# Kernel tuning notes

Measured on AMD Instinct MI355X. Metric: run time of the kernel, lower is better.

Reference implementation:

```python
import jax, jax.numpy as jnp
import numpy as np

N, NFEAT, NHID, NCLASS, NHEADS = 4096, 512, 64, 40, 8
ALPHA = 0.2  # LeakyReLU negative slope
NEG_BIG = -9e15


def _xavier(key, shape, gain=1.414):
    fan_in, fan_out = shape[0], shape[1]
    bound = gain * np.sqrt(6.0 / (fan_in + fan_out))
    return jax.random.uniform(key, shape, jnp.float32, -bound, bound)


def setup_inputs() -> dict:
    key = jax.random.key(0)
    ks = jax.random.split(key, 6)
    x = jax.random.normal(ks[0], (N, NFEAT), jnp.float32)
    adj = jax.random.randint(ks[1], (N, N), 0, 2).astype(jnp.float32)
    # per-head params of the 8 input GAT layers
    Ws = _xavier(ks[2], (NHEADS, NFEAT, NHID))          # stacked W: [H, F, D]
    a_s = _xavier(ks[3], (NHEADS, 2 * NHID, 1))[..., 0]  # [H, 2D]
    # output GAT layer (concat=False)
    W_out = _xavier(ks[4], (NHID * NHEADS, NCLASS))
    a_out = _xavier(ks[5], (2 * NCLASS, 1))[..., 0]      # [2C]
    return {"x": x, "adj": adj, "Ws": Ws, "a_s": a_s, "W_out": W_out, "a_out": a_out}


def _gat_layer(inp, adj_mask, W, a, concat):
    # h = inp @ W : [N, D]
    h = inp @ W
    D = h.shape[1]
    a1, a2 = a[:D], a[D:]
    # e[i,j] = leakyrelu(a . [h_i, h_j]) = leakyrelu(h_i.a1 + h_j.a2)
    # (same math as the N*N*2D concat in the original, without materializing it)
    f1 = h @ a1  # [N]
    f2 = h @ a2  # [N]
    e = jax.nn.leaky_relu(f1[:, None] + f2[None, :], negative_slope=ALPHA)
    att = jax.nn.softmax(jnp.where(adj_mask, e, NEG_BIG), axis=1)
    h_prime = att @ h  # [N, D]
    return jax.nn.elu(h_prime) if concat else h_prime


def reference(x, adj, Ws, a_s, W_out, a_out):
    adj_mask = adj > 0
    # 8 attention heads over the input features (eval mode: dropout is identity)
    heads = jax.vmap(lambda W, a: _gat_layer(x, adj_mask, W, a, True))(Ws, a_s)  # [H, N, D]
    x2 = jnp.transpose(heads, (1, 0, 2)).reshape(N, NHEADS * NHID)  # concat along feature dim
    out = _gat_layer(x2, adj_mask, W_out, a_out, False)  # [N, C]
    out = jax.nn.elu(out)
    return jax.nn.log_softmax(out, axis=1)
```

## Files before the change

### kernel.cpp

```cpp
#include <hip/hip_runtime.h>
#include <hip/hip_bf16.h>
#include <stdint.h>

#define NN 4096
#define NF 512
#define NH 64
#define NCLS 40
#define NHEADS 8
#define LOG2E 1.4426950408889634f

typedef __attribute__((ext_vector_type(8))) short bh8;
typedef __attribute__((ext_vector_type(4))) float f32x4;

__device__ __forceinline__ unsigned short f2bu(float f) {
    union { float f; unsigned u; } v; v.f = f;
    unsigned r = (v.u + 0x7FFFu + ((v.u >> 16) & 1u)) >> 16;
    return (unsigned short)r;
}
__device__ __forceinline__ float lrelu(float x) { return fmaxf(x, 0.2f * x); }
__device__ __forceinline__ float elu1(float x) { return x > 0.f ? x : expm1f(x); }
__device__ __forceinline__ float exp2fast(float x) {
    float r; asm("v_exp_f32 %0, %1" : "=v"(r) : "v"(x)); return r;
}
__device__ __forceinline__ unsigned fenc(float f) {
    unsigned u = __builtin_bit_cast(unsigned, f);
    return ((int)u < 0) ? ~u : (u | 0x80000000u);
}
__device__ __forceinline__ float fdec(unsigned k) {
    unsigned u = (k & 0x80000000u) ? (k ^ 0x80000000u) : ~k;
    return __builtin_bit_cast(float, u);
}
__device__ __forceinline__ int sbfe1(unsigned v, int off) {
#if __has_builtin(__builtin_amdgcn_sbfe)
    return __builtin_amdgcn_sbfe((int)v, off, 1);
#else
    return ((int)(v << (31 - off))) >> 31;
#endif
}
__device__ __forceinline__ float bmask(float p, unsigned mdw, int bit) {
    return __builtin_bit_cast(float,
        __builtin_bit_cast(unsigned, p) & (unsigned)sbfe1(mdw, bit));
}
__device__ __forceinline__ unsigned pack2(float x, float y) {
    unsigned ux = __builtin_bit_cast(unsigned, x), uy = __builtin_bit_cast(unsigned, y);
    ux += 0x7FFFu + ((ux >> 16) & 1u);
    uy += 0x7FFFu + ((uy >> 16) & 1u);
    return __builtin_amdgcn_perm(uy, ux, 0x07060302u);
}

__global__ __launch_bounds__(256) void prep_all_k(const float* __restrict__ x,
                                                  const float* __restrict__ adj,
                                                  const float* __restrict__ Ws,
                                                  const float* __restrict__ Wo,
                                                  unsigned short* __restrict__ xb,
                                                  unsigned short* __restrict__ WT,
                                                  unsigned short* __restrict__ WoT,
                                                  unsigned char* __restrict__ adjp,
                                                  unsigned* __restrict__ FM1u,
                                                  unsigned* __restrict__ FM2u) {
    const int bid = blockIdx.x, tid = threadIdx.x;
    if (bid < 8192) {
        __shared__ unsigned char sm[4][64];
        const int i = bid >> 1, half = bid & 1;
        const float* rp = adj + (size_t)i * NN + half * 2048 + tid * 8;
        float4 v0 = ((const float4*)rp)[0];
        float4 v1 = ((const float4*)rp)[1];
        unsigned b = (v0.x > 0.f ? 1u : 0u) | (v0.y > 0.f ? 2u : 0u) |
                     (v0.z > 0.f ? 4u : 0u) | (v0.w > 0.f ? 8u : 0u) |
                     (v1.x > 0.f ? 16u : 0u) | (v1.y > 0.f ? 32u : 0u) |
                     (v1.z > 0.f ? 64u : 0u) | (v1.w > 0.f ? 128u : 0u);
        sm[tid & 3][tid >> 2] = (unsigned char)b;
        __syncthreads();
        if (tid < 64) {
            int gp = tid >> 4, word = tid & 15;
            unsigned d = *(const unsigned*)&sm[gp][word * 4];
            *(unsigned*)(adjp + ((size_t)i * 4 + gp) * 128 + half * 64 + word * 4) = d;
        }
    } else if (bid < 10240) {
        if (bid == 8192) {
            if (tid < 8) FM1u[tid] = 0u;
            if (tid == 8) FM2u[0] = 0u;
        }
        int t = (bid - 8192) * 256 + tid;
        float4 v = ((const float4*)x)[t];
        uint2 o; o.x = pack2(v.x, v.y); o.y = pack2(v.z, v.w);
        ((uint2*)xb)[t] = o;
    } else if (bid < 11264) {
        int j = (bid - 10240) * 256 + tid;
        int c = j >> 9, k = j & 511;
        WT[j] = f2bu(Ws[(size_t)(c >> 6) * (NF * NH) + (size_t)k * NH + (c & 63)]);
    } else {
        int j = (bid - 11264) * 256 + tid;
        int c = j >> 9, k = j & 511;
        WoT[j] = f2bu(c < NCLS ? Wo[(size_t)k * NCLS + c] : 0.f);
    }
}

__global__ __launch_bounds__(512) void gemm1_k(const unsigned short* __restrict__ xb,
                                               const unsigned short* __restrict__ WT,
                                               const float* __restrict__ a_s,
                                               unsigned short* __restrict__ Bp1,
                                               float* __restrict__ f1L,
                                               float* __restrict__ f2L,
                                               unsigned* __restrict__ FM1u) {
    __shared__ unsigned short xs[128 * 40];
    __shared__ unsigned short wsm[64 * 40];
    const int tid = threadIdx.x;
    const int w = tid >> 6, lane = tid & 63, r16 = lane & 15, grp = lane >> 4;
    const int i0 = blockIdx.x << 7, h = blockIdx.y, c0 = h << 6;
    const int srow = tid >> 2, sseg = tid & 3;
    const unsigned short* xsrc = xb + (size_t)(i0 + srow) * NF + sseg * 8;
    const unsigned short* wsrc = WT + (size_t)(c0 + (srow & 63)) * NF + sseg * 8;
    f32x4 a0 = {0,0,0,0}, a1 = {0,0,0,0}, a2 = {0,0,0,0}, a3 = {0,0,0,0};
    bh8 rx = *(const bh8*)(xsrc);
    bh8 rw; if (tid < 256) rw = *(const bh8*)(wsrc);
    for (int kb = 0; kb < NF; kb += 32) {
        *(bh8*)(xs + srow * 40 + sseg * 8) = rx;
        if (tid < 256) *(bh8*)(wsm + srow * 40 + sseg * 8) = rw;
        __syncthreads();
        if (kb + 32 < NF) {
            rx = *(const bh8*)(xsrc + kb + 32);
            if (tid < 256) rw = *(const bh8*)(wsrc + kb + 32);
        }
        bh8 af = *(const bh8*)(xs + (w * 16 + r16) * 40 + grp * 8);
        bh8 b0 = *(const bh8*)(wsm + (r16) * 40 + grp * 8);
        bh8 b1 = *(const bh8*)(wsm + (16 + r16) * 40 + grp * 8);
        bh8 b2 = *(const bh8*)(wsm + (32 + r16) * 40 + grp * 8);
        bh8 b3 = *(const bh8*)(wsm + (48 + r16) * 40 + grp * 8);
        a0 = __builtin_amdgcn_mfma_f32_16x16x32_bf16(af, b0, a0, 0, 0, 0);
        a1 = __builtin_amdgcn_mfma_f32_16x16x32_bf16(af, b1, a1, 0, 0, 0);
        a2 = __builtin_amdgcn_mfma_f32_16x16x32_bf16(af, b2, a2, 0, 0, 0);
        a3 = __builtin_amdgcn_mfma_f32_16x16x32_bf16(af, b3, a3, 0, 0, 0);
        __syncthreads();
    }
    const int jt = (i0 >> 5) + (w >> 1);
    const int kg = ((w & 1) << 1) + (grp >> 1);
    const int lanep = kg * 16 + r16;
    const int ebase = (grp & 1) * 4;
    unsigned short* bp = Bp1 + ((size_t)(h * 128 + jt)) * 2048 + lanep * 8 + ebase;
    {
        uint2 v;
        v.x = pack2(a0[0], a0[1]); v.y = pack2(a0[2], a0[3]); *(uint2*)(bp + 0 * 512) = v;
        v.x = pack2(a1[0], a1[1]); v.y = pack2(a1[2], a1[3]); *(uint2*)(bp + 1 * 512) = v;
        v.x = pack2(a2[0], a2[1]); v.y = pack2(a2[2], a2[3]); *(uint2*)(bp + 2 * 512) = v;
        v.x = pack2(a3[0], a3[1]); v.y = pack2(a3[2], a3[3]); *(uint2*)(bp + 3 * 512) = v;
    }
    const float* ap = a_s + h * 128;
    float a1v[4], a2v[4];
#pragma unroll
    for (int n = 0; n < 4; ++n) { a1v[n] = ap[r16 + 16 * n]; a2v[n] = ap[64 + r16 + 16 * n]; }
    float wmax = -3.0e38f;
#pragma unroll
    for (int r = 0; r < 4; ++r) {
        const int orow = i0 + w * 16 + grp * 4 + r;
        float s1 = a0[r] * a1v[0] + a1[r] * a1v[1] + a2[r] * a1v[2] + a3[r] * a1v[3];
        float s2 = a0[r] * a2v[0] + a1[r] * a2v[1] + a2[r] * a2v[2] + a3[r] * a2v[3];
#pragma unroll
        for (int o2 = 1; o2 < 16; o2 <<= 1) { s1 += __shfl_xor(s1, o2); s2 += __shfl_xor(s2, o2); }
        s1 *= LOG2E; s2 *= LOG2E;
        if (r16 == 0) { f1L[h * NN + orow] = s1; f2L[h * NN + orow] = s2; }
        wmax = fmaxf(wmax, s2);
    }
    wmax = fmaxf(wmax, __shfl_xor(wmax, 16));
    wmax = fmaxf(wmax, __shfl_xor(wmax, 32));
    if (lane == 0) atomicMax(&FM1u[h], fenc(wmax));
}

__global__ __launch_bounds__(256) void gemm2_k(const unsigned short* __restrict__ x2b,
                                               const unsigned short* __restrict__ WoT,
                                               const float* __restrict__ a_out,
                                               unsigned short* __restrict__ Bp2,
                                               float* __restrict__ f12L,
                                               float* __restrict__ f22L,
                                               unsigned* __restrict__ FM2u) {
    __shared__ unsigned short xs[64 * 40];
    __shared__ unsigned short wsm[48 * 40];
    const int tid = threadIdx.x;
    const int w = tid >> 6, lane = tid & 63, r16 = lane & 15, grp = lane >> 4;
    const int i0 = blockIdx.x << 6;
    const int srow = tid >> 2, sseg = tid & 3;
    const unsigned short* xsrc = x2b + (size_t)(i0 + srow) * NF + sseg * 8;
    const unsigned short* wsrc = WoT + (size_t)srow * NF + sseg * 8;
    f32x4 a0 = {0,0,0,0}, a1 = {0,0,0,0}, a2 = {0,0,0,0};
    bh8 rx = *(const bh8*)(xsrc);
    bh8 rw; if (tid < 192) rw = *(const bh8*)(wsrc);
    for (int kb = 0; kb < NF; kb += 32) {
        *(bh8*)(xs + srow * 40 + sseg * 8) = rx;
        if (tid < 192) *(bh8*)(wsm + srow * 40 + sseg * 8) = rw;
        __syncthreads();
        if (kb + 32 < NF) {
            rx = *(const bh8*)(xsrc + kb + 32);
            if (tid < 192) rw = *(const bh8*)(wsrc + kb + 32);
        }
        bh8 af = *(const bh8*)(xs + (w * 16 + r16) * 40 + grp * 8);
        bh8 b0 = *(const bh8*)(wsm + (r16) * 40 + grp * 8);
        bh8 b1 = *(const bh8*)(wsm + (16 + r16) * 40 + grp * 8);
        bh8 b2 = *(const bh8*)(wsm + (32 + r16) * 40 + grp * 8);
        a0 = __builtin_amdgcn_mfma_f32_16x16x32_bf16(af, b0, a0, 0, 0, 0);
        a1 = __builtin_amdgcn_mfma_f32_16x16x32_bf16(af, b1, a1, 0, 0, 0);
        a2 = __builtin_amdgcn_mfma_f32_16x16x32_bf16(af, b2, a2, 0, 0, 0);
        __syncthreads();
    }
    const int jt = (i0 >> 5) + (w >> 1);
    const int kg = ((w & 1) << 1) + (grp >> 1);
    const int lanep = kg * 16 + r16;
    const int ebase = (grp & 1) * 4;
    unsigned short* bp = Bp2 + (size_t)jt * 1536 + lanep * 8 + ebase;
    {
        uint2 v;
        v.x = pack2(a0[0], a0[1]); v.y = pack2(a0[2], a0[3]); *(uint2*)(bp + 0 * 512) = v;
        v.x = pack2(a1[0], a1[1]); v.y = pack2(a1[2], a1[3]); *(uint2*)(bp + 1 * 512) = v;
        v.x = pack2(a2[0], a2[1]); v.y = pack2(a2[2], a2[3]); *(uint2*)(bp + 2 * 512) = v;
    }
    float a1v[3], a2v[3];
#pragma unroll
    for (int n = 0; n < 3; ++n) {
        int col = r16 + 16 * n;
        a1v[n] = col < NCLS ? a_out[col] : 0.f;
        a2v[n] = col < NCLS ? a_out[NCLS + col] : 0.f;
    }
    float wmax = -3.0e38f;
#pragma unroll
    for (int r = 0; r < 4; ++r) {
        const int orow = i0 + w * 16 + grp * 4 + r;
        float s1 = a0[r] * a1v[0] + a1[r] * a1v[1] + a2[r] * a1v[2];
        float s2 = a0[r] * a2v[0] + a1[r] * a2v[1] + a2[r] * a2v[2];
#pragma unroll
        for (int o2 = 1; o2 < 16; o2 <<= 1) { s1 += __shfl_xor(s1, o2); s2 += __shfl_xor(s2, o2); }
        s1 *= LOG2E; s2 *= LOG2E;
        if (r16 == 0) { f12L[orow] = s1; f22L[orow] = s2; }
        wmax = fmaxf(wmax, s2);
    }
    wmax = fmaxf(wmax, __shfl_xor(wmax, 16));
    wmax = fmaxf(wmax, __shfl_xor(wmax, 32));
    if (lane == 0) atomicMax(&FM2u[0], fenc(wmax));
}

__global__ __launch_bounds__(512, 4) void attn1_k(const unsigned short* __restrict__ Bp1,
                                                  const unsigned char* __restrict__ adjp,
                                                  const float* __restrict__ f1L,
                                                  const float* __restrict__ f2L,
                                                  const unsigned* __restrict__ FM1u,
                                                  unsigned short* __restrict__ x2b) {
    __shared__ float EFs[8192];
    __shared__ unsigned ADJd[64 * 4 * 33];
    const int tid = threadIdx.x, w = tid >> 6, lane = tid & 63;
    const int r16 = lane & 15, grp = lane >> 4;
    const int rowg = w & 3, jq = w >> 2;
    const int h = blockIdx.y;
    const int i0 = blockIdx.x * 64;
    const float fm = fdec(FM1u[h]);
    const float* f2p = f2L + h * NN;
    for (int t = 0; t < 8; ++t) {
        int j = tid + t * 512;
        float d = f2p[j] - fm;
        EFs[2 * j] = exp2fast(d);
        EFs[2 * j + 1] = exp2fast(0.2f * d);
    }
    {
        const unsigned* asrc = (const unsigned*)(adjp + (size_t)i0 * 512);
        for (int t = 0; t < 16; ++t) {
            int idx = tid + t * 512;
            ADJd[(idx >> 5) * 33 + (idx & 31)] = asrc[idx];
        }
    }
    const int irow = i0 + rowg * 16 + r16;
    const float f1v = f1L[h * NN + irow];
    const float mL = lrelu(f1v + fm);
    const float A = exp2fast(f1v + fm - mL);
    const float B = exp2fast(__builtin_fmaf(0.2f, f1v + fm, -mL));
    __syncthreads();
    const unsigned* adjrd = ADJd + ((rowg * 16 + r16) * 4 + grp) * 33 + jq * 16;
    const float* efp = EFs + grp * 16;
    const unsigned short* Bbase = Bp1 + (size_t)h * 128 * 2048 + lane * 8;
    f32x4 acc0 = {0,0,0,0}, acc1 = {0,0,0,0}, acc2 = {0,0,0,0}, acc3 = {0,0,0,0}, accd = {0,0,0,0};
    const short ov = (r16 == 0) ? (short)0x3F80 : (short)0;
    bh8 ones;
#pragma unroll
    for (int e = 0; e < 8; ++e) ones[e] = ov;
    bh8 nb0, nb1, nb2, nb3;
#define PREF1(JT) { const unsigned short* Bn = Bbase + (size_t)(JT) * 2048;              \
        nb0 = *(const bh8*)(Bn);        nb1 = *(const bh8*)(Bn + 512);                    \
        nb2 = *(const bh8*)(Bn + 1024); nb3 = *(const bh8*)(Bn + 1536); }
    const int jtbase = jq * 64;
    PREF1(jtbase);
    for (int jt4 = 0; jt4 < 16; ++jt4) {
        const unsigned mdw = adjrd[jt4];
#pragma unroll
        for (int u = 0; u < 4; ++u) {
            const int jt = jtbase + jt4 * 4 + u;
            bh8 b0 = nb0, b1 = nb1, b2 = nb2, b3 = nb3;
            PREF1(jt + 1);
            const float* e4 = efp + jt * 64;
            float4 ea = *(const float4*)(e4);
            float4 eb = *(const float4*)(e4 + 4);
            float4 ec = *(const float4*)(e4 + 8);
            float4 ed = *(const float4*)(e4 + 12);
            const int bb = u * 8;
            union { bh8 v; unsigned u32[4]; } pk;
            {
                float p0 = bmask(fmaxf(A * ea.x, B * ea.y), mdw, bb + 0);
                float p1 = bmask(fmaxf(A * ea.z, B * ea.w), mdw, bb + 1);
                pk.u32[0] = __builtin_amdgcn_perm(__builtin_bit_cast(unsigned, p1),
                                                  __builtin_bit_cast(unsigned, p0), 0x07060302u);
                float p2 = bmask(fmaxf(A * eb.x, B * eb.y), mdw, bb + 2);
                float p3 = bmask(fmaxf(A * eb.z, B * eb.w), mdw, bb + 3);
                pk.u32[1] = __builtin_amdgcn_perm(__builtin_bit_cast(unsigned, p3),
                                                  __builtin_bit_cast(unsigned, p2), 0x07060302u);
                float p4 = bmask(fmaxf(A * ec.x, B * ec.y), mdw, bb + 4);
                float p5 = bmask(fmaxf(A * ec.z, B * ec.w), mdw, bb + 5);
                pk.u32[2] = __builtin_amdgcn_perm(__builtin_bit_cast(unsigned, p5),
                                                  __builtin_bit_cast(unsigned, p4), 0x07060302u);
                float p6 = bmask(fmaxf(A * ed.x, B * ed.y), mdw, bb + 6);
                float p7 = bmask(fmaxf(A * ed.z, B * ed.w), mdw, bb + 7);
                pk.u32[3] = __builtin_amdgcn_perm(__builtin_bit_cast(unsigned, p7),
                                                  __builtin_bit_cast(unsigned, p6), 0x07060302u);
            }
            acc0 = __builtin_amdgcn_mfma_f32_16x16x32_bf16(pk.v, b0, acc0, 0, 0, 0);
            acc1 = __builtin_amdgcn_mfma_f32_16x16x32_bf16(pk.v, b1, acc1, 0, 0, 0);
            acc2 = __builtin_amdgcn_mfma_f32_16x16x32_bf16(pk.v, b2, acc2, 0, 0, 0);
            acc3 = __builtin_amdgcn_mfma_f32_16x16x32_bf16(pk.v, b3, acc3, 0, 0, 0);
            accd = __builtin_amdgcn_mfma_f32_16x16x32_bf16(pk.v, ones, accd, 0, 0, 0);
        }
    }
#undef PREF1
    __syncthreads();
    float (*comb)[64][21] = (float(*)[64][21])EFs;
    if (jq == 1) {
        float* cb = &comb[rowg][lane][0];
#pragma unroll
        for (int r = 0; r < 4; ++r) {
            cb[r] = acc0[r]; cb[4 + r] = acc1[r]; cb[8 + r] = acc2[r];
            cb[12 + r] = acc3[r]; cb[16 + r] = accd[r];
        }
    }
    __syncthreads();
    if (jq == 0) {
        const float* cb = &comb[rowg][lane][0];
#pragma unroll
        for (int r = 0; r < 4; ++r) {
            acc0[r] += cb[r]; acc1[r] += cb[4 + r]; acc2[r] += cb[8 + r];
            acc3[r] += cb[12 + r]; accd[r] += cb[16 + r];
        }
#pragma unroll
        for (int r = 0; r < 4; ++r) {
            const float den = __shfl(accd[r], lane & 48);
            const float inv = 1.0f / den;
            unsigned short* o = x2b + (size_t)(i0 + rowg * 16 + grp * 4 + r) * NF + h * 64 + r16;
            o[0]  = f2bu(elu1(acc0[r] * inv));
            o[16] = f2bu(elu1(acc1[r] * inv));
            o[32] = f2bu(elu1(acc2[r] * inv));
            o[48] = f2bu(elu1(acc3[r] * inv));
        }
    }
}

__global__ __launch_bounds__(512, 6) void attn2_k(const unsigned short* __restrict__ Bp2,
                                                  const unsigned char* __restrict__ adjp,
                                                  const float* __restrict__ f12L,
                                                  const float* __restrict__ f22L,
                                                  const unsigned* __restrict__ FM2u,
                                                  float* __restrict__ out) {
    __shared__ float EFs[8192];
    __shared__ float comb[8][64][17];
    const int tid = threadIdx.x, w = tid >> 6, lane = tid & 63;
    const int r16 = lane & 15, grp = lane >> 4;
    const int i0 = blockIdx.x * 16;
    const int i = i0 + r16;
    const float fm = fdec(FM2u[0]);
    for (int t = 0; t < 8; ++t) {
        int j = tid + t * 512;
        float d = f22L[j] - fm;
        EFs[2 * j] = exp2fast(d);
        EFs[2 * j + 1] = exp2fast(0.2f * d);
    }
    const float f1v = f12L[i];
    const float mL = lrelu(f1v + fm);
    const float A = exp2fast(f1v + fm - mL);
    const float B = exp2fast(__builtin_fmaf(0.2f, f1v + fm, -mL));
    __syncthreads();
    const int jt0 = w * 16;
    const uint4 a4 = *(const uint4*)(adjp + ((size_t)i * 4 + grp) * 128 + jt0);
    f32x4 acc0 = {0,0,0,0}, acc1 = {0,0,0,0}, acc2 = {0,0,0,0}, accd = {0,0,0,0};
    const short ov = (r16 == 0) ? (short)0x3F80 : (short)0;
    bh8 ones;
#pragma unroll
    for (int e = 0; e < 8; ++e) ones[e] = ov;
    const unsigned short* Bbase = Bp2 + lane * 8;
    const float* efp = EFs + grp * 16;
    bh8 nb0, nb1, nb2;
#define PREF2(JT) { const unsigned short* Bn = Bbase + (size_t)(JT) * 1536;              \
        nb0 = *(const bh8*)(Bn); nb1 = *(const bh8*)(Bn + 512); nb2 = *(const bh8*)(Bn + 1024); }
    PREF2(jt0);
#pragma unroll
    for (int q = 0; q < 4; ++q) {
        const unsigned mdw = (q == 0) ? a4.x : (q == 1) ? a4.y : (q == 2) ? a4.z : a4.w;
#pragma unroll
        for (int u = 0; u < 4; ++u) {
            const int jt = jt0 + q * 4 + u;
            bh8 b0 = nb0, b1 = nb1, b2 = nb2;
            PREF2(jt + 1);
            const float* e4 = efp + jt * 64;
            float4 ea = *(const float4*)(e4);
            float4 eb = *(const float4*)(e4 + 4);
            float4 ec = *(const float4*)(e4 + 8);
            float4 ed = *(const float4*)(e4 + 12);
            const int bb = u * 8;
            union { bh8 v; unsigned u32[4]; } pk;
            {
                float p0 = bmask(fmaxf(A * ea.x, B * ea.y), mdw, bb + 0);
                float p1 = bmask(fmaxf(A * ea.z, B * ea.w), mdw, bb + 1);
                pk.u32[0] = __builtin_amdgcn_perm(__builtin_bit_cast(unsigned, p1),
                                                  __builtin_bit_cast(unsigned, p0), 0x07060302u);
                float p2 = bmask(fmaxf(A * eb.x, B * eb.y), mdw, bb + 2);
                float p3 = bmask(fmaxf(A * eb.z, B * eb.w), mdw, bb + 3);
                pk.u32[1] = __builtin_amdgcn_perm(__builtin_bit_cast(unsigned, p3),
                                                  __builtin_bit_cast(unsigned, p2), 0x07060302u);
                float p4 = bmask(fmaxf(A * ec.x, B * ec.y), mdw, bb + 4);
                float p5 = bmask(fmaxf(A * ec.z, B * ec.w), mdw, bb + 5);
                pk.u32[2] = __builtin_amdgcn_perm(__builtin_bit_cast(unsigned, p5),
                                                  __builtin_bit_cast(unsigned, p4), 0x07060302u);
                float p6 = bmask(fmaxf(A * ed.x, B * ed.y), mdw, bb + 6);
                float p7 = bmask(fmaxf(A * ed.z, B * ed.w), mdw, bb + 7);
                pk.u32[3] = __builtin_amdgcn_perm(__builtin_bit_cast(unsigned, p7),
                                                  __builtin_bit_cast(unsigned, p6), 0x07060302u);
            }
            acc0 = __builtin_amdgcn_mfma_f32_16x16x32_bf16(pk.v, b0, acc0, 0, 0, 0);
            acc1 = __builtin_amdgcn_mfma_f32_16x16x32_bf16(pk.v, b1, acc1, 0, 0, 0);
            acc2 = __builtin_amdgcn_mfma_f32_16x16x32_bf16(pk.v, b2, acc2, 0, 0, 0);
            accd = __builtin_amdgcn_mfma_f32_16x16x32_bf16(pk.v, ones, accd, 0, 0, 0);
        }
    }
#undef PREF2
    {
        float* cb = &comb[w][lane][0];
#pragma unroll
        for (int r = 0; r < 4; ++r) {
            cb[r] = acc0[r]; cb[4 + r] = acc1[r]; cb[8 + r] = acc2[r]; cb[12 + r] = accd[r];
        }
    }
    __syncthreads();
    if (w < 4) {
        const float* sb = &comb[w + 4][lane][0];
        float* cb = &comb[w][lane][0];
#pragma unroll
        for (int r = 0; r < 4; ++r) {
            acc0[r] += sb[r]; acc1[r] += sb[4 + r]; acc2[r] += sb[8 + r]; accd[r] += sb[12 + r];
            cb[r] = acc0[r]; cb[4 + r] = acc1[r]; cb[8 + r] = acc2[r]; cb[12 + r] = accd[r];
        }
    }
    __syncthreads();
    if (w < 2) {
        const float* sb = &comb[w + 2][lane][0];
        float* cb = &comb[w][lane][0];
#pragma unroll
        for (int r = 0; r < 4; ++r) {
            acc0[r] += sb[r]; acc1[r] += sb[4 + r]; acc2[r] += sb[8 + r]; accd[r] += sb[12 + r];
            cb[r] = acc0[r]; cb[4 + r] = acc1[r]; cb[8 + r] = acc2[r]; cb[12 + r] = accd[r];
        }
    }
    __syncthreads();
    if (w == 0) {
        const float* sb = &comb[1][lane][0];
#pragma unroll
        for (int r = 0; r < 4; ++r) {
            acc0[r] += sb[r]; acc1[r] += sb[4 + r]; acc2[r] += sb[8 + r]; accd[r] += sb[12 + r];
        }
#pragma unroll
        for (int r = 0; r < 4; ++r) {
            const int row = grp * 4 + r;
            const float den = __shfl(accd[r], lane & 48);
            const float inv = 1.0f / den;
            float v0 = elu1(acc0[r] * inv);
            float v1 = elu1(acc1[r] * inv);
            float v2 = (r16 < 8) ? elu1(acc2[r] * inv) : -3.0e38f;
            float mx = fmaxf(fmaxf(v0, v1), v2);
#pragma unroll
            for (int o = 1; o < 16; o <<= 1) mx = fmaxf(mx, __shfl_xor(mx, o));
            float ex = __expf(v0 - mx) + __expf(v1 - mx) + ((r16 < 8) ? __expf(v2 - mx) : 0.f);
#pragma unroll
            for (int o = 1; o < 16; o <<= 1) ex += __shfl_xor(ex, o);
            const float lse = mx + logf(ex);
            float* op = out + (size_t)(i0 + row) * NCLS;
            op[r16] = v0 - lse;
            op[16 + r16] = v1 - lse;
            if (r16 < 8) op[32 + r16] = v2 - lse;
        }
    }
}

#define OFF_XB   0ULL
#define OFF_WT   4194304ULL
#define OFF_WOT  4718592ULL
#define OFF_BP1  4767744ULL
#define OFF_X2B  8962048ULL
#define OFF_BP2  13156352ULL
#define OFF_F1L  13549568ULL
#define OFF_F2L  13680640ULL
#define OFF_F12  13811712ULL
#define OFF_F22  13828096ULL
#define OFF_FM1  13844480ULL
#define OFF_FM2  13844736ULL
#define OFF_ADJ  13844992ULL

extern "C" void kernel_launch(void* const* d_in, const int* in_sizes, int n_in,
                              void* d_out, int out_size, void* d_ws, size_t ws_size,
                              hipStream_t stream) {
    const float* x     = (const float*)d_in[0];
    const float* adj   = (const float*)d_in[1];
    const float* Ws    = (const float*)d_in[2];
    const float* a_s   = (const float*)d_in[3];
    const float* W_out = (const float*)d_in[4];
    const float* a_out = (const float*)d_in[5];
    float* out = (float*)d_out;
    char* w = (char*)d_ws;

    unsigned short* xb  = (unsigned short*)(w + OFF_XB);
    unsigned short* WT  = (unsigned short*)(w + OFF_WT);
    unsigned short* WoT = (unsigned short*)(w + OFF_WOT);
    unsigned short* Bp1 = (unsigned short*)(w + OFF_BP1);
    unsigned short* x2b = (unsigned short*)(w + OFF_X2B);
    unsigned short* Bp2 = (unsigned short*)(w + OFF_BP2);
    float* f1L = (float*)(w + OFF_F1L);
    float* f2L = (float*)(w + OFF_F2L);
    float* f12 = (float*)(w + OFF_F12);
    float* f22 = (float*)(w + OFF_F22);
    unsigned* FM1u = (unsigned*)(w + OFF_FM1);
    unsigned* FM2u = (unsigned*)(w + OFF_FM2);
    unsigned char* adjp = (unsigned char*)(w + OFF_ADJ);

    prep_all_k<<<11360, 256, 0, stream>>>(x, adj, Ws, W_out, xb, WT, WoT, adjp, FM1u, FM2u);
    gemm1_k<<<dim3(32, 8), 512, 0, stream>>>(xb, WT, a_s, Bp1, f1L, f2L, FM1u);
    attn1_k<<<dim3(64, 8), 512, 0, stream>>>(Bp1, adjp, f1L, f2L, FM1u, x2b);
    gemm2_k<<<64, 256, 0, stream>>>(x2b, WoT, a_out, Bp2, f12, f22, FM2u);
    attn2_k<<<256, 512, 0, stream>>>(Bp2, adjp, f12, f22, FM2u, out);
}
```

Baseline: 195.1 us.

## Double-buffer GEMM shared tiles, deepen attention B prefetch, widen adj packing

Both GEMM kernels now use double-buffered shared-memory tiles. The next K-slice is written into the alternate buffer after the MFMAs, which removes one barrier per iteration. The attention kernel prefetches B fragments two tiles ahead using alternating register sets, aiming to hide more global latency at the cost of extra registers. The adjacency bit-packing now handles a full row per block with 16 floats per thread, halving the block count of the prep kernel.

```diff
diff --git a/kernel.cpp b/kernel.cpp
--- a/kernel.cpp
+++ b/kernel.cpp
@@ -59,38 +59,45 @@
                                                   unsigned* __restrict__ FM1u,
                                                   unsigned* __restrict__ FM2u) {
     const int bid = blockIdx.x, tid = threadIdx.x;
-    if (bid < 8192) {
-        __shared__ unsigned char sm[4][64];
-        const int i = bid >> 1, half = bid & 1;
-        const float* rp = adj + (size_t)i * NN + half * 2048 + tid * 8;
+    if (bid < 4096) {
+        __shared__ unsigned char sm[4][128];
+        const int i = bid;
+        const float* rp = adj + (size_t)i * NN + tid * 16;
         float4 v0 = ((const float4*)rp)[0];
         float4 v1 = ((const float4*)rp)[1];
-        unsigned b = (v0.x > 0.f ? 1u : 0u) | (v0.y > 0.f ? 2u : 0u) |
-                     (v0.z > 0.f ? 4u : 0u) | (v0.w > 0.f ? 8u : 0u) |
-                     (v1.x > 0.f ? 16u : 0u) | (v1.y > 0.f ? 32u : 0u) |
-                     (v1.z > 0.f ? 64u : 0u) | (v1.w > 0.f ? 128u : 0u);
-        sm[tid & 3][tid >> 2] = (unsigned char)b;
+        float4 v2 = ((const float4*)rp)[2];
+        float4 v3 = ((const float4*)rp)[3];
+        unsigned b0 = (v0.x > 0.f ? 1u : 0u) | (v0.y > 0.f ? 2u : 0u) |
+                      (v0.z > 0.f ? 4u : 0u) | (v0.w > 0.f ? 8u : 0u) |
+                      (v1.x > 0.f ? 16u : 0u) | (v1.y > 0.f ? 32u : 0u) |
+                      (v1.z > 0.f ? 64u : 0u) | (v1.w > 0.f ? 128u : 0u);
+        unsigned b1 = (v2.x > 0.f ? 1u : 0u) | (v2.y > 0.f ? 2u : 0u) |
+                      (v2.z > 0.f ? 4u : 0u) | (v2.w > 0.f ? 8u : 0u) |
+                      (v3.x > 0.f ? 16u : 0u) | (v3.y > 0.f ? 32u : 0u) |
+                      (v3.z > 0.f ? 64u : 0u) | (v3.w > 0.f ? 128u : 0u);
+        sm[(tid & 1) * 2][tid >> 1] = (unsigned char)b0;
+        sm[(tid & 1) * 2 + 1][tid >> 1] = (unsigned char)b1;
         __syncthreads();
-        if (tid < 64) {
-            int gp = tid >> 4, word = tid & 15;
+        if (tid < 128) {
+            int gp = tid >> 5, word = tid & 31;
             unsigned d = *(const unsigned*)&sm[gp][word * 4];
-            *(unsigned*)(adjp + ((size_t)i * 4 + gp) * 128 + half * 64 + word * 4) = d;
-        }
-    } else if (bid < 10240) {
-        if (bid == 8192) {
+            *(unsigned*)(adjp + ((size_t)i * 4 + gp) * 128 + word * 4) = d;
+        }
+    } else if (bid < 6144) {
+        if (bid == 4096) {
             if (tid < 8) FM1u[tid] = 0u;
             if (tid == 8) FM2u[0] = 0u;
         }
-        int t = (bid - 8192) * 256 + tid;
+        int t = (bid - 4096) * 256 + tid;
         float4 v = ((const float4*)x)[t];
         uint2 o; o.x = pack2(v.x, v.y); o.y = pack2(v.z, v.w);
         ((uint2*)xb)[t] = o;
-    } else if (bid < 11264) {
-        int j = (bid - 10240) * 256 + tid;
+    } else if (bid < 7168) {
+        int j = (bid - 6144) * 256 + tid;
         int c = j >> 9, k = j & 511;
         WT[j] = f2bu(Ws[(size_t)(c >> 6) * (NF * NH) + (size_t)k * NH + (c & 63)]);
     } else {
-        int j = (bid - 11264) * 256 + tid;
+        int j = (bid - 7168) * 256 + tid;
         int c = j >> 9, k = j & 511;
         WoT[j] = f2bu(c < NCLS ? Wo[(size_t)k * NCLS + c] : 0.f);
     }
@@ -103,8 +110,8 @@
                                                float* __restrict__ f1L,
                                                float* __restrict__ f2L,
                                                unsigned* __restrict__ FM1u) {
-    __shared__ unsigned short xs[128 * 40];
-    __shared__ unsigned short wsm[64 * 40];
+    __shared__ unsigned short xs[2][128 * 40];
+    __shared__ unsigned short wsm[2][64 * 40];
     const int tid = threadIdx.x;
     const int w = tid >> 6, lane = tid & 63, r16 = lane & 15, grp = lane >> 4;
     const int i0 = blockIdx.x << 7, h = blockIdx.y, c0 = h << 6;
@@ -114,23 +121,28 @@
     f32x4 a0 = {0,0,0,0}, a1 = {0,0,0,0}, a2 = {0,0,0,0}, a3 = {0,0,0,0};
     bh8 rx = *(const bh8*)(xsrc);
     bh8 rw; if (tid < 256) rw = *(const bh8*)(wsrc);
-    for (int kb = 0; kb < NF; kb += 32) {
-        *(bh8*)(xs + srow * 40 + sseg * 8) = rx;
-        if (tid < 256) *(bh8*)(wsm + srow * 40 + sseg * 8) = rw;
-        __syncthreads();
-        if (kb + 32 < NF) {
-            rx = *(const bh8*)(xsrc + kb + 32);
-            if (tid < 256) rw = *(const bh8*)(wsrc + kb + 32);
-        }
-        bh8 af = *(const bh8*)(xs + (w * 16 + r16) * 40 + grp * 8);
-        bh8 b0 = *(const bh8*)(wsm + (r16) * 40 + grp * 8);
-        bh8 b1 = *(const bh8*)(wsm + (16 + r16) * 40 + grp * 8);
-        bh8 b2 = *(const bh8*)(wsm + (32 + r16) * 40 + grp * 8);
-        bh8 b3 = *(const bh8*)(wsm + (48 + r16) * 40 + grp * 8);
+    *(bh8*)(&xs[0][srow * 40 + sseg * 8]) = rx;
+    if (tid < 256) *(bh8*)(&wsm[0][srow * 40 + sseg * 8]) = rw;
+    __syncthreads();
+    for (int kb = 0; kb < 16; ++kb) {
+        const int cur = kb & 1;
+        if (kb < 15) {
+            rx = *(const bh8*)(xsrc + (kb + 1) * 32);
+            if (tid < 256) rw = *(const bh8*)(wsrc + (kb + 1) * 32);
+        }
+        bh8 af = *(const bh8*)(&xs[cur][(w * 16 + r16) * 40 + grp * 8]);
+        bh8 b0 = *(const bh8*)(&wsm[cur][(r16) * 40 + grp * 8]);
+        bh8 b1 = *(const bh8*)(&wsm[cur][(16 + r16) * 40 + grp * 8]);
+        bh8 b2 = *(const bh8*)(&wsm[cur][(32 + r16) * 40 + grp * 8]);
+        bh8 b3 = *(const bh8*)(&wsm[cur][(48 + r16) * 40 + grp * 8]);
         a0 = __builtin_amdgcn_mfma_f32_16x16x32_bf16(af, b0, a0, 0, 0, 0);
         a1 = __builtin_amdgcn_mfma_f32_16x16x32_bf16(af, b1, a1, 0, 0, 0);
         a2 = __builtin_amdgcn_mfma_f32_16x16x32_bf16(af, b2, a2, 0, 0, 0);
         a3 = __builtin_amdgcn_mfma_f32_16x16x32_bf16(af, b3, a3, 0, 0, 0);
+        if (kb < 15) {
+            *(bh8*)(&xs[cur ^ 1][srow * 40 + sseg * 8]) = rx;
+            if (tid < 256) *(bh8*)(&wsm[cur ^ 1][srow * 40 + sseg * 8]) = rw;
+        }
         __syncthreads();
     }
     const int jt = (i0 >> 5) + (w >> 1);
@@ -173,8 +185,8 @@
                                                float* __restrict__ f12L,
                                                float* __restrict__ f22L,
                                                unsigned* __restrict__ FM2u) {
-    __shared__ unsigned short xs[64 * 40];
-    __shared__ unsigned short wsm[48 * 40];
+    __shared__ unsigned short xs[2][64 * 40];
+    __shared__ unsigned short wsm[2][48 * 40];
     const int tid = threadIdx.x;
     const int w = tid >> 6, lane = tid & 63, r16 = lane & 15, grp = lane >> 4;
     const int i0 = blockIdx.x << 6;
@@ -184,21 +196,26 @@
     f32x4 a0 = {0,0,0,0}, a1 = {0,0,0,0}, a2 = {0,0,0,0};
     bh8 rx = *(const bh8*)(xsrc);
     bh8 rw; if (tid < 192) rw = *(const bh8*)(wsrc);
-    for (int kb = 0; kb < NF; kb += 32) {
-        *(bh8*)(xs + srow * 40 + sseg * 8) = rx;
-        if (tid < 192) *(bh8*)(wsm + srow * 40 + sseg * 8) = rw;
-        __syncthreads();
-        if (kb + 32 < NF) {
-            rx = *(const bh8*)(xsrc + kb + 32);
-            if (tid < 192) rw = *(const bh8*)(wsrc + kb + 32);
-        }
-        bh8 af = *(const bh8*)(xs + (w * 16 + r16) * 40 + grp * 8);
-        bh8 b0 = *(const bh8*)(wsm + (r16) * 40 + grp * 8);
-        bh8 b1 = *(const bh8*)(wsm + (16 + r16) * 40 + grp * 8);
-        bh8 b2 = *(const bh8*)(wsm + (32 + r16) * 40 + grp * 8);
+    *(bh8*)(&xs[0][srow * 40 + sseg * 8]) = rx;
+    if (tid < 192) *(bh8*)(&wsm[0][srow * 40 + sseg * 8]) = rw;
+    __syncthreads();
+    for (int kb = 0; kb < 16; ++kb) {
+        const int cur = kb & 1;
+        if (kb < 15) {
+            rx = *(const bh8*)(xsrc + (kb + 1) * 32);
+            if (tid < 192) rw = *(const bh8*)(wsrc + (kb + 1) * 32);
+        }
+        bh8 af = *(const bh8*)(&xs[cur][(w * 16 + r16) * 40 + grp * 8]);
+        bh8 b0 = *(const bh8*)(&wsm[cur][(r16) * 40 + grp * 8]);
+        bh8 b1 = *(const bh8*)(&wsm[cur][(16 + r16) * 40 + grp * 8]);
+        bh8 b2 = *(const bh8*)(&wsm[cur][(32 + r16) * 40 + grp * 8]);
         a0 = __builtin_amdgcn_mfma_f32_16x16x32_bf16(af, b0, a0, 0, 0, 0);
         a1 = __builtin_amdgcn_mfma_f32_16x16x32_bf16(af, b1, a1, 0, 0, 0);
         a2 = __builtin_amdgcn_mfma_f32_16x16x32_bf16(af, b2, a2, 0, 0, 0);
+        if (kb < 15) {
+            *(bh8*)(&xs[cur ^ 1][srow * 40 + sseg * 8]) = rx;
+            if (tid < 192) *(bh8*)(&wsm[cur ^ 1][srow * 40 + sseg * 8]) = rw;
+        }
         __syncthreads();
     }
     const int jt = (i0 >> 5) + (w >> 1);
@@ -278,19 +295,24 @@
     bh8 ones;
 #pragma unroll
     for (int e = 0; e < 8; ++e) ones[e] = ov;
-    bh8 nb0, nb1, nb2, nb3;
-#define PREF1(JT) { const unsigned short* Bn = Bbase + (size_t)(JT) * 2048;              \
-        nb0 = *(const bh8*)(Bn);        nb1 = *(const bh8*)(Bn + 512);                    \
-        nb2 = *(const bh8*)(Bn + 1024); nb3 = *(const bh8*)(Bn + 1536); }
+    bh8 pa0, pa1, pa2, pa3, pb0, pb1, pb2, pb3;
+#define PREFA(JT) { const unsigned short* Bn = Bbase + (size_t)(JT) * 2048;              \
+        pa0 = *(const bh8*)(Bn);        pa1 = *(const bh8*)(Bn + 512);                    \
+        pa2 = *(const bh8*)(Bn + 1024); pa3 = *(const bh8*)(Bn + 1536); }
+#define PREFB(JT) { const unsigned short* Bn = Bbase + (size_t)(JT) * 2048;              \
+        pb0 = *(const bh8*)(Bn);        pb1 = *(const bh8*)(Bn + 512);                    \
+        pb2 = *(const bh8*)(Bn + 1024); pb3 = *(const bh8*)(Bn + 1536); }
     const int jtbase = jq * 64;
-    PREF1(jtbase);
+    PREFA(jtbase);
+    PREFB(jtbase + 1);
     for (int jt4 = 0; jt4 < 16; ++jt4) {
         const unsigned mdw = adjrd[jt4];
 #pragma unroll
         for (int u = 0; u < 4; ++u) {
             const int jt = jtbase + jt4 * 4 + u;
-            bh8 b0 = nb0, b1 = nb1, b2 = nb2, b3 = nb3;
-            PREF1(jt + 1);
+            bh8 b0, b1, b2, b3;
+            if ((u & 1) == 0) { b0 = pa0; b1 = pa1; b2 = pa2; b3 = pa3; PREFA((jt + 2) & 127); }
+            else              { b0 = pb0; b1 = pb1; b2 = pb2; b3 = pb3; PREFB((jt + 2) & 127); }
             const float* e4 = efp + jt * 64;
             float4 ea = *(const float4*)(e4);
             float4 eb = *(const float4*)(e4 + 4);
@@ -323,7 +345,8 @@
             accd = __builtin_amdgcn_mfma_f32_16x16x32_bf16(pk.v, ones, accd, 0, 0, 0);
         }
     }
-#undef PREF1
+#undef PREFA
+#undef PREFB
     __syncthreads();
     float (*comb)[64][21] = (float(*)[64][21])EFs;
     if (jq == 1) {
@@ -529,7 +552,7 @@
     unsigned* FM2u = (unsigned*)(w + OFF_FM2);
     unsigned char* adjp = (unsigned char*)(w + OFF_ADJ);
 
-    prep_all_k<<<11360, 256, 0, stream>>>(x, adj, Ws, W_out, xb, WT, WoT, adjp, FM1u, FM2u);
+    prep_all_k<<<7264, 256, 0, stream>>>(x, adj, Ws, W_out, xb, WT, WoT, adjp, FM1u, FM2u);
     gemm1_k<<<dim3(32, 8), 512, 0, stream>>>(xb, WT, a_s, Bp1, f1L, f2L, FM1u);
     attn1_k<<<dim3(64, 8), 512, 0, stream>>>(Bp1, adjp, f1L, f2L, FM1u, x2b);
     gemm2_k<<<64, 256, 0, stream>>>(x2b, WoT, a_out, Bp2, f12, f22, FM2u);
```

New measurement: 199.6 us. +2.3%, slower.
